# Kernel tuning notes

Hardware: AMD Instinct MI355X
Metric: run time of the kernel (lower is better)

Reference implementation:

```python
import jax, jax.numpy as jnp
import numpy as np

D_MODEL = 1024
D_HIDDEN = 4096
D_OUT = 1024
N_EXPERTS = 8
TOP_K = 2
LOAD_BALANCE_WEIGHT = 0.01


def setup_inputs() -> dict:
    key = jax.random.key(0)
    ks = jax.random.split(key, 8)
    s = 0.02
    return {
        "input_tensor": jax.random.normal(ks[0], (4, 2048, D_MODEL), dtype=jnp.float32),
        "router_w": jax.random.normal(ks[1], (N_EXPERTS, D_MODEL), dtype=jnp.float32) * s,
        "router_b": jnp.zeros((N_EXPERTS,), dtype=jnp.float32),
        "w1": jax.random.normal(ks[2], (N_EXPERTS, D_HIDDEN, D_MODEL), dtype=jnp.float32) * s,
        "b1": jnp.zeros((N_EXPERTS, D_HIDDEN), dtype=jnp.float32),
        "w2": jax.random.normal(ks[3], (N_EXPERTS, D_OUT, D_HIDDEN), dtype=jnp.float32) * s,
        "b2": jnp.zeros((N_EXPERTS, D_OUT), dtype=jnp.float32),
    }


def _moe(input_tensor, router_w, router_b, w1, b1, w2, b2):
    B, S, D = input_tensor.shape
    x = input_tensor.reshape(-1, D)  # [T, D]
    T = x.shape[0]

    router_logits = x @ router_w.T + router_b          # [T, E]
    router_probs = jax.nn.softmax(router_logits, -1)   # [T, E]
    topk_w, topk_idx = jax.lax.top_k(router_probs, TOP_K)  # [T, K]
    topk_w = topk_w / jnp.sum(topk_w, axis=-1, keepdims=True)

    # Dense combine weights: zero for unselected experts (same math as
    # gather/scatter loop since unselected contributions get weight 0).
    combine = jnp.zeros((T, N_EXPERTS), dtype=topk_w.dtype)
    combine = combine.at[jnp.arange(T)[:, None], topk_idx].add(topk_w)  # [T, E]

    out = jnp.zeros((T, D_OUT), dtype=x.dtype)
    for e in range(N_EXPERTS):  # fixed, small expert loop
        h = jax.nn.relu(x @ w1[e].T + b1[e])      # [T, H]
        y = h @ w2[e].T + b2[e]                   # [T, O]
        out = out + combine[:, e:e + 1] * y
    output = out.reshape(B, S, D_OUT)

    # Load-balance loss
    one_hot = jax.nn.one_hot(topk_idx, N_EXPERTS, dtype=router_probs.dtype)  # [T, K, E]
    usage_frac = jnp.sum(one_hot, axis=(0, 1)) / (T * TOP_K)                 # [E]
    mean_prob = jnp.mean(router_probs, axis=0)                               # [E]
    lb_loss = LOAD_BALANCE_WEIGHT * N_EXPERTS * jnp.sum(usage_frac * mean_prob)
    return output, lb_loss


def reference(input_tensor, router_w, router_b, w1, b1, w2, b2):
    return _moe(input_tensor, router_w, router_b, w1, b1, w2, b2)
```

## Files before the change

kernel.cpp:

```cpp
#include <hip/hip_runtime.h>

typedef unsigned short u16;
typedef __bf16 bf16x8 __attribute__((ext_vector_type(8)));
typedef float f32x4 __attribute__((ext_vector_type(4)));

#define T_TOKENS 8192
#define DM 1024
#define DH 4096
#define DO 1024
#define NE 8

#define XB_OFF   0ull
#define W1B_OFF  16777216ull
#define W2B_OFF  16777216ull
#define H_OFF    83886080ull
#define PT_OFF   218103808ull
#define PG_OFF   218169344ull
#define TI_OFF   218234880ull
#define TG_OFF   218300416ull
#define ST_OFF   218365952ull
#define YW_OFF   218370048ull
#define YW_SZ    67108864ull

typedef __attribute__((address_space(3))) void lds_void;
typedef __attribute__((address_space(1))) const void gbl_void;

__device__ __forceinline__ void gload_lds16(const void* g, void* l) {
  __builtin_amdgcn_global_load_lds((gbl_void*)g, (lds_void*)l, 16, 0, 0);
}

__device__ __forceinline__ u16 f2bf(float f) {
  union { float f; unsigned u; } a; a.f = f;
  unsigned u = a.u;
  return (u16)((u + 0x7FFFu + ((u >> 16) & 1u)) >> 16);
}

__global__ __launch_bounds__(256) void cast_f32_bf16(const float* __restrict__ src,
                                                     u16* __restrict__ dst, int n4) {
  int i = blockIdx.x * 256 + threadIdx.x;
  if (i >= n4) return;
  float4 v = ((const float4*)src)[i];
  ushort4 o;
  o.x = f2bf(v.x); o.y = f2bf(v.y); o.z = f2bf(v.z); o.w = f2bf(v.w);
  ((ushort4*)dst)[i] = o;
}

__global__ __launch_bounds__(256) void router_kernel(
    const float* __restrict__ x, const float* __restrict__ rw,
    const float* __restrict__ rb,
    int* __restrict__ tidx, float* __restrict__ tgate,
    int* __restrict__ counts, float* __restrict__ psum)
{
  __shared__ float srw[NE * DM];
  __shared__ float s_psum[NE];
  __shared__ int s_cnt[NE];

  for (int i = threadIdx.x; i < NE * DM; i += 256) srw[i] = rw[i];
  if (threadIdx.x < NE) { s_psum[threadIdx.x] = 0.f; s_cnt[threadIdx.x] = 0; }
  __syncthreads();

  const int wave = threadIdx.x >> 6;
  const int lane = threadIdx.x & 63;
  const int t = blockIdx.x * 4 + wave;

  float xv[16];
#pragma unroll
  for (int i = 0; i < 16; i++) xv[i] = x[(size_t)t * DM + i * 64 + lane];

  float logits[8];
#pragma unroll
  for (int e = 0; e < 8; e++) {
    float p = 0.f;
#pragma unroll
    for (int i = 0; i < 16; i++) p += xv[i] * srw[e * DM + i * 64 + lane];
#pragma unroll
    for (int o = 32; o > 0; o >>= 1) p += __shfl_xor(p, o, 64);
    logits[e] = p;
  }

  if (lane == 0) {
    float pe[8];
    float mx = -1e30f;
    for (int e = 0; e < 8; e++) { logits[e] += rb[e]; mx = fmaxf(mx, logits[e]); }
    float s = 0.f;
    for (int e = 0; e < 8; e++) { pe[e] = expf(logits[e] - mx); s += pe[e]; }
    float inv = 1.f / s;
    for (int e = 0; e < 8; e++) { pe[e] *= inv; atomicAdd(&s_psum[e], pe[e]); }
    int i0 = 0;
    for (int e = 1; e < 8; e++) if (pe[e] > pe[i0]) i0 = e;
    int i1 = (i0 == 0) ? 1 : 0;
    for (int e = 0; e < 8; e++) if (e != i0 && pe[e] > pe[i1]) i1 = e;
    float g = pe[i0] + pe[i1];
    tidx[t * 2] = i0; tidx[t * 2 + 1] = i1;
    tgate[t * 2] = pe[i0] / g; tgate[t * 2 + 1] = pe[i1] / g;
    atomicAdd(&s_cnt[i0], 1); atomicAdd(&s_cnt[i1], 1);
  }
  __syncthreads();
  if (threadIdx.x < NE) {
    atomicAdd(&counts[threadIdx.x], s_cnt[threadIdx.x]);
    atomicAdd(&psum[threadIdx.x], s_psum[threadIdx.x]);
  }
}

__global__ void offsets_kernel(const int* __restrict__ counts, int* __restrict__ offs) {
  if (threadIdx.x == 0) {
    int a = 0;
    for (int e = 0; e < NE; e++) { offs[e] = a; a += counts[e]; }
  }
}

__global__ __launch_bounds__(256) void scatter_kernel(
    const int* tidx, const float* __restrict__ tgate,
    const int* __restrict__ offs, int* __restrict__ cursor,
    int* __restrict__ ptok, float* __restrict__ pgate, int* ppos)
{
  int t = blockIdx.x * 256 + threadIdx.x;
  int e0 = tidx[t * 2], e1 = tidx[t * 2 + 1];
  float g0 = tgate[t * 2], g1 = tgate[t * 2 + 1];
  int p0 = offs[e0] + atomicAdd(&cursor[e0], 1);
  int p1 = offs[e1] + atomicAdd(&cursor[e1], 1);
  ptok[p0] = t; pgate[p0] = g0;
  ptok[p1] = t; pgate[p1] = g1;
  ppos[t * 2] = p0; ppos[t * 2 + 1] = p1;
}


#define FENCE asm volatile("" ::: "memory")
#define BAR  do { FENCE; __builtin_amdgcn_s_barrier(); FENCE; } while (0)
#define VMW4 asm volatile("s_waitcnt vmcnt(4)" ::: "memory")
#define VMW0 asm volatile("s_waitcnt vmcnt(0)" ::: "memory")

#define G256_DECLS                                                             \
  __shared__ __align__(16) u16 sm[65536];                         \
  const int tid = threadIdx.x;                                                 \
  const int lane = tid & 63;                                                   \
  const int wave = tid >> 6;                                                   \
  const int wm = wave & 1, wn = wave >> 1;                                     \
  const int q = lane >> 4, ml = lane & 15;                                     \
  const int swz0 = (q ^ (ml & 7)) * 8;             \
  const int swz1 = ((4 + q) ^ (ml & 7)) * 8;                   \
  const int baseA = wm * 8192 + ml * 64;                                       \
  const int baseB = 16384 + (wn >> 1) * 8192 + (wn & 1) * 4096 + ml * 64;      \
  const int cs = ((tid & 7) ^ ((tid >> 3) & 7)) * 8;    \
  const int srow = tid >> 3;          \
  f32x4 acc[8][4];                                                             \
  { const f32x4 z_ = {0.f, 0.f, 0.f, 0.f};                                     \
    _Pragma("unroll") for (int i_ = 0; i_ < 8; i_++)                           \
      _Pragma("unroll") for (int j_ = 0; j_ < 4; j_++) acc[i_][j_] = z_; }     \
  bf16x8 areg[4][2], breg[4][2];

#define STAGE_A(buf, half, k0)                                                 \
  { u16* d_ = sm + (buf) * 32768 + (half) * 8192 + tid * 8;                    \
    gload_lds16(aP[half][0] + (k0), d_);                                       \
    gload_lds16(aP[half][1] + (k0), d_ + 4096); }

#define STAGE_B(buf, half, k0, KD)                                             \
  { u16* d_ = sm + (buf) * 32768 + 16384 + (half) * 8192 + tid * 8;            \
    gload_lds16(bB + (size_t)((half) * 128) * (KD) + (k0), d_);                \
    gload_lds16(bB + (size_t)((half) * 128 + 64) * (KD) + (k0), d_ + 4096); }

#define READ_A(buf, mh)                                                        \
  _Pragma("unroll") for (int m_ = 0; m_ < 4; m_++) {                           \
    areg[m_][0] = *(const bf16x8*)&sm[(buf) * 32768 + baseA +                  \
                                      ((mh) * 4 + m_) * 1024 + swz0];          \
    areg[m_][1] = *(const bf16x8*)&sm[(buf) * 32768 + baseA +                  \
                                      ((mh) * 4 + m_) * 1024 + swz1];          \
  }

#define READ_B(buf, nh)                                                        \
  _Pragma("unroll") for (int n_ = 0; n_ < 2; n_++) {                           \
    breg[(nh) * 2 + n_][0] = *(const bf16x8*)&sm[(buf) * 32768 + baseB +       \
                                      ((nh) * 2 + n_) * 1024 + swz0];          \
    breg[(nh) * 2 + n_][1] = *(const bf16x8*)&sm[(buf) * 32768 + baseB +       \
                                      ((nh) * 2 + n_) * 1024 + swz1];          \
  }

#define MFMA_Q(mh, nh)                                                         \
  __builtin_amdgcn_s_setprio(1);                                               \
  _Pragma("unroll") for (int m_ = 0; m_ < 4; m_++)                             \
    _Pragma("unroll") for (int n_ = 0; n_ < 2; n_++) {                         \
      acc[(mh)*4+m_][(nh)*2+n_] = __builtin_amdgcn_mfma_f32_16x16x32_bf16(     \
          areg[m_][0], breg[(nh)*2+n_][0], acc[(mh)*4+m_][(nh)*2+n_], 0,0,0);  \
      acc[(mh)*4+m_][(nh)*2+n_] = __builtin_amdgcn_mfma_f32_16x16x32_bf16(     \
          areg[m_][1], breg[(nh)*2+n_][1], acc[(mh)*4+m_][(nh)*2+n_], 0,0,0);  \
    }                                                                          \
  __builtin_amdgcn_s_setprio(0);

#define G256_ITER(KD, k1, k2, k3, ST)                                          \
  READ_A(0, 0) READ_B(0, 0)                                                    \
  STAGE_A(1, 1, (k1))                                                          \
  BAR; MFMA_Q(0, 0) BAR;                                                       \
  READ_B(0, 1)                                                                 \
  STAGE_B(1, 1, (k1), KD)                                                      \
  BAR; MFMA_Q(0, 1) BAR;                                                       \
  READ_A(0, 1)                                                                 \
  if (ST) STAGE_B(0, 0, (k2), KD)                                              \
  BAR; MFMA_Q(1, 1) BAR;                                                       \
  if (ST) STAGE_A(0, 0, (k2))                                                  \
  BAR; MFMA_Q(1, 0)                                                            \
  if (ST) { VMW4; } else { VMW0; }                                             \
  BAR;                                                                         \
  READ_A(1, 0) READ_B(1, 0)                                                    \
  if (ST) STAGE_A(0, 1, (k2))                                                  \
  BAR; MFMA_Q(0, 0) BAR;                                                       \
  READ_B(1, 1)                                                                 \
  if (ST) STAGE_B(0, 1, (k2), KD)                                              \
  BAR; MFMA_Q(0, 1) BAR;                                                       \
  READ_A(1, 1)                                                                 \
  if (ST) STAGE_B(1, 0, (k3), KD)                                              \
  BAR; MFMA_Q(1, 1) BAR;                                                       \
  if (ST) STAGE_A(1, 0, (k3))                                                  \
  BAR; MFMA_Q(1, 0)                                                            \
  if (ST) { VMW4; }                                                            \
  BAR;

#define G256_KLOOP(KD)                                                         \
  STAGE_B(0, 0, 0, KD) STAGE_A(0, 0, 0)                                        \
  STAGE_A(0, 1, 0) STAGE_B(0, 1, 0, KD)                                        \
  STAGE_B(1, 0, 64, KD) STAGE_A(1, 0, 64)                                      \
  VMW4; BAR;                                                                   \
  for (int it_ = 0; it_ < (KD) / 128 - 1; ++it_) {                             \
    const int kb_ = it_ * 128;                                                 \
    G256_ITER(KD, kb_ + 64, kb_ + 128, kb_ + 192, 1)                           \
  }                                                                            \
  G256_ITER(KD, (KD) - 64, 0, 0, 0)

__global__ __launch_bounds__(512, 2) void gemm1_kernel(
    const u16* __restrict__ xb, const u16* __restrict__ w1b,
    const float* __restrict__ b1, const int* __restrict__ ptok,
    const int* __restrict__ offs, const int* __restrict__ counts,
    u16* __restrict__ h)
{
  const int e = blockIdx.z;
  const int cnt = counts[e];
  const int row0 = blockIdx.y * 256;
  if (row0 >= cnt) return;
  const int off = offs[e];
  const int col0 = blockIdx.x * 256;

  G256_DECLS

  const u16* aP[2][2];
#pragma unroll
  for (int a_ = 0; a_ < 2; a_++)
#pragma unroll
    for (int j_ = 0; j_ < 2; j_++) {
      int p = row0 + a_ * 128 + srow + j_ * 64;
      int tk = ptok[off + (p < cnt ? p : 0)];
      aP[a_][j_] = xb + (size_t)tk * DM + cs;
    }
  const u16* bB = w1b + ((size_t)e * DH + col0 + srow) * DM + cs;

  G256_KLOOP(DM)

#pragma unroll
  for (int M = 0; M < 8; M++) {
#pragma unroll
    for (int r_ = 0; r_ < 4; r_++) {
      int prow = row0 + wm * 128 + M * 16 + q * 4 + r_;
      if (prow < cnt) {
#pragma unroll
        for (int N = 0; N < 4; N++) {
          int gcol = col0 + wn * 64 + N * 16 + ml;
          float v = acc[M][N][r_] + b1[e * DH + gcol];
          h[(size_t)(off + prow) * DH + gcol] = f2bf(fmaxf(v, 0.f));
        }
      }
    }
  }
}

__global__ __launch_bounds__(512, 2) void gemm2_kernel(
    const u16* __restrict__ h, const u16* __restrict__ w2b,
    const float* __restrict__ b2, const int* __restrict__ ptok,
    const float* __restrict__ pgate,
    const int* __restrict__ offs, const int* __restrict__ counts,
    float* __restrict__ yw, float* __restrict__ out, int use_yw)
{
  const int e = blockIdx.z;
  const int cnt = counts[e];
  const int row0 = blockIdx.y * 256;
  if (row0 >= cnt) return;
  const int off = offs[e];
  const int col0 = blockIdx.x * 256;

  G256_DECLS

  const u16* aP[2][2];
#pragma unroll
  for (int a_ = 0; a_ < 2; a_++)
#pragma unroll
    for (int j_ = 0; j_ < 2; j_++) {
      int p = row0 + a_ * 128 + srow + j_ * 64;
      aP[a_][j_] = h + (size_t)(off + (p < cnt ? p : 0)) * DH + cs;
    }
  const u16* bB = w2b + ((size_t)e * DO + col0 + srow) * DH + cs;

  G256_KLOOP(DH)

#pragma unroll
  for (int M = 0; M < 8; M++) {
#pragma unroll
    for (int r_ = 0; r_ < 4; r_++) {
      int prow = row0 + wm * 128 + M * 16 + q * 4 + r_;
      if (prow < cnt) {
        int pr = off + prow;
        float g = pgate[pr];
        if (use_yw) {
#pragma unroll
          for (int N = 0; N < 4; N++) {
            int gcol = col0 + wn * 64 + N * 16 + ml;
            yw[(size_t)pr * DO + gcol] = g * (acc[M][N][r_] + b2[e * DO + gcol]);
          }
        } else {
          int t = ptok[pr];
#pragma unroll
          for (int N = 0; N < 4; N++) {
            int gcol = col0 + wn * 64 + N * 16 + ml;
            atomicAdd(&out[(size_t)t * DO + gcol], g * (acc[M][N][r_] + b2[e * DO + gcol]));
          }
        }
      }
    }
  }
}

__global__ __launch_bounds__(256) void combine_kernel(
    const float* __restrict__ yw, const int* __restrict__ ppos,
    float* __restrict__ out)
{
  int t = blockIdx.x;
  int j = threadIdx.x;
  int p0 = ppos[t * 2], p1 = ppos[t * 2 + 1];
  float4 a = ((const float4*)(yw + (size_t)p0 * DO))[j];
  float4 b = ((const float4*)(yw + (size_t)p1 * DO))[j];
  float4 o;
  o.x = a.x + b.x; o.y = a.y + b.y; o.z = a.z + b.z; o.w = a.w + b.w;
  ((float4*)(out + (size_t)t * DO))[j] = o;
}

__global__ void loss_kernel(const int* __restrict__ counts, const float* __restrict__ psum,
                            float* __restrict__ out, size_t idx, int T) {
  if (threadIdx.x == 0 && blockIdx.x == 0) {
    float s = 0.f;
    for (int e = 0; e < NE; e++)
      s += ((float)counts[e] / (float)(T * 2)) * (psum[e] / (float)T);
    out[idx] = 0.01f * 8.0f * s;
  }
}

extern "C" void kernel_launch(void* const* d_in, const int* in_sizes, int n_in,
                              void* d_out, int out_size, void* d_ws, size_t ws_size,
                              hipStream_t stream) {
  const float* x  = (const float*)d_in[0];
  const float* rw = (const float*)d_in[1];
  const float* rb = (const float*)d_in[2];
  const float* w1 = (const float*)d_in[3];
  const float* b1 = (const float*)d_in[4];
  const float* w2 = (const float*)d_in[5];
  const float* b2 = (const float*)d_in[6];
  float* out = (float*)d_out;
  char* ws = (char*)d_ws;

  u16* xb    = (u16*)(ws + XB_OFF);
  u16* w1b   = (u16*)(ws + W1B_OFF);
  u16* w2b   = (u16*)(ws + W2B_OFF);
  u16* h     = (u16*)(ws + H_OFF);
  int* ptok  = (int*)(ws + PT_OFF);
  float* pgate = (float*)(ws + PG_OFF);
  int* tidx  = (int*)(ws + TI_OFF);
  float* tgate = (float*)(ws + TG_OFF);
  int* counts = (int*)(ws + ST_OFF);
  int* cursor = (int*)(ws + ST_OFF + 32);
  int* offs   = (int*)(ws + ST_OFF + 64);
  float* psum = (float*)(ws + ST_OFF + 96);
  int* ppos   = tidx;
  float* yw   = (float*)(ws + YW_OFF);

  const bool use_yw = ws_size >= YW_OFF + YW_SZ;

  if (!use_yw)
    hipMemsetAsync(d_out, 0, (size_t)out_size * sizeof(float), stream);
  hipMemsetAsync(ws + ST_OFF, 0, 256, stream);

  cast_f32_bf16<<<(T_TOKENS * DM / 4 + 255) / 256, 256, 0, stream>>>(x, xb, T_TOKENS * DM / 4);
  cast_f32_bf16<<<(NE * DH * DM / 4 + 255) / 256, 256, 0, stream>>>(w1, w1b, NE * DH * DM / 4);

  router_kernel<<<T_TOKENS / 4, 256, 0, stream>>>(x, rw, rb, tidx, tgate, counts, psum);
  offsets_kernel<<<1, 64, 0, stream>>>(counts, offs);
  scatter_kernel<<<T_TOKENS / 256, 256, 0, stream>>>(tidx, tgate, offs, cursor, ptok, pgate, ppos);

  gemm1_kernel<<<dim3(DH / 256, 32, NE), 512, 0, stream>>>(xb, w1b, b1, ptok, offs, counts, h);

  cast_f32_bf16<<<(NE * DO * DH / 4 + 255) / 256, 256, 0, stream>>>(w2, w2b, NE * DO * DH / 4);

  gemm2_kernel<<<dim3(DO / 256, 32, NE), 512, 0, stream>>>(
      h, w2b, b2, ptok, pgate, offs, counts, yw, out, use_yw ? 1 : 0);

  if (use_yw)
    combine_kernel<<<T_TOKENS, 256, 0, stream>>>(yw, ppos, out);

  loss_kernel<<<1, 1, 0, stream>>>(counts, psum, out, (size_t)out_size - 1, T_TOKENS);
}
```

Baseline: 837.0 us.

## Fuse both expert GEMMs into a persistent kernel with per-row-tile dependency flags

Replaces the separate gemm1 and gemm2 launches with one persistent kernel of 256 blocks that pulls tiles from a global atomic counter. GEMM1 tiles are handed out first. GEMM2 tiles spin-wait on per-(expert, row-tile) completion counters, so second-layer work on finished rows can overlap with the tail of the first layer. The w2 bf16 copy moves to its own workspace region so it can be cast before the fused kernel without overwriting w1b. This removes the kernel boundary and the wave-quantization tail between the two GEMMs, at the cost of spin-waiting and a larger workspace requirement. If the workspace is too small it falls back to the original path.

```diff
diff --git a/kernel.cpp b/kernel.cpp
--- a/kernel.cpp
+++ b/kernel.cpp
@@ -19,7 +19,9 @@
 #define TI_OFF   218234880ull
 #define TG_OFF   218300416ull
 #define ST_OFF   218365952ull
-#define YW_OFF   218370048ull
+#define W2X_OFF  218370048ull
+#define W2X_SZ   67108864ull
+#define YW_OFF   285478912ull
 #define YW_SZ    67108864ull
 
 typedef __attribute__((address_space(3))) void lds_void;
@@ -130,8 +132,7 @@
 #define VMW4 asm volatile("s_waitcnt vmcnt(4)" ::: "memory")
 #define VMW0 asm volatile("s_waitcnt vmcnt(0)" ::: "memory")
 
-#define G256_DECLS                                                             \
-  __shared__ __align__(16) u16 sm[65536];                         \
+#define G256_IDS                                                               \
   const int tid = threadIdx.x;                                                 \
   const int lane = tid & 63;                                                   \
   const int wave = tid >> 6;                                                   \
@@ -142,12 +143,12 @@
   const int baseA = wm * 8192 + ml * 64;                                       \
   const int baseB = 16384 + (wn >> 1) * 8192 + (wn & 1) * 4096 + ml * 64;      \
   const int cs = ((tid & 7) ^ ((tid >> 3) & 7)) * 8;    \
-  const int srow = tid >> 3;          \
-  f32x4 acc[8][4];                                                             \
+  const int srow = tid >> 3;
+
+#define G256_ACC_ZERO                                                          \
   { const f32x4 z_ = {0.f, 0.f, 0.f, 0.f};                                     \
     _Pragma("unroll") for (int i_ = 0; i_ < 8; i_++)                           \
-      _Pragma("unroll") for (int j_ = 0; j_ < 4; j_++) acc[i_][j_] = z_; }     \
-  bf16x8 areg[4][2], breg[4][2];
+      _Pragma("unroll") for (int j_ = 0; j_ < 4; j_++) acc[i_][j_] = z_; }
 
 #define STAGE_A(buf, half, k0)                                                 \
   { u16* d_ = sm + (buf) * 32768 + (half) * 8192 + tid * 8;                    \
@@ -225,6 +226,135 @@
   }                                                                            \
   G256_ITER(KD, (KD) - 64, 0, 0, 0)
 
+__global__ __launch_bounds__(512, 2) void moe_mlp_fused(
+    const u16* __restrict__ xb, const u16* __restrict__ w1b,
+    const float* __restrict__ b1, const u16* __restrict__ w2b,
+    const float* __restrict__ b2, const int* __restrict__ ptok,
+    const float* __restrict__ pgate, const int* __restrict__ offs,
+    const int* __restrict__ counts, u16* __restrict__ hbuf,
+    float* __restrict__ yw, float* out, int* done, int* gctr, int use_yw)
+{
+  __shared__ __align__(16) u16 sm[65536];
+  __shared__ int s_tk;
+  G256_IDS
+  f32x4 acc[8][4];
+  bf16x8 areg[4][2], breg[4][2];
+
+  int rt[NE];
+  int n1 = 0, n2 = 0;
+#pragma unroll
+  for (int e_ = 0; e_ < NE; e_++) {
+    rt[e_] = (counts[e_] + 255) >> 8;
+    n1 += rt[e_] * 16;
+    n2 += rt[e_] * 4;
+  }
+
+  for (;;) {
+    __syncthreads();
+    if (tid == 0) s_tk = atomicAdd(gctr, 1);
+    __syncthreads();
+    const int tk = s_tk;
+    if (tk >= n1 + n2) break;
+
+    int e = 0, idx, ry, cx, g2;
+    if (tk < n1) {
+      g2 = 0; idx = tk;
+      while (idx >= rt[e] * 16) { idx -= rt[e] * 16; e++; }
+      ry = idx >> 4; cx = idx & 15;
+    } else {
+      g2 = 1; idx = tk - n1;
+      while (idx >= rt[e] * 4) { idx -= rt[e] * 4; e++; }
+      ry = idx >> 2; cx = idx & 3;
+    }
+    const int cnt = counts[e], off = offs[e];
+    const int row0 = ry * 256, col0 = cx * 256;
+
+    G256_ACC_ZERO
+
+    if (!g2) {
+      const u16* aP[2][2];
+#pragma unroll
+      for (int a_ = 0; a_ < 2; a_++)
+#pragma unroll
+        for (int j_ = 0; j_ < 2; j_++) {
+          int p = row0 + a_ * 128 + srow + j_ * 64;
+          int tkn = ptok[off + (p < cnt ? p : row0)];
+          aP[a_][j_] = xb + (size_t)tkn * DM + cs;
+        }
+      const u16* bB = w1b + ((size_t)e * DH + col0 + srow) * DM + cs;
+
+      G256_KLOOP(DM)
+
+#pragma unroll
+      for (int M = 0; M < 8; M++) {
+#pragma unroll
+        for (int r_ = 0; r_ < 4; r_++) {
+          int prow = row0 + wm * 128 + M * 16 + q * 4 + r_;
+          if (prow < cnt) {
+#pragma unroll
+            for (int N = 0; N < 4; N++) {
+              int gcol = col0 + wn * 64 + N * 16 + ml;
+              float v = acc[M][N][r_] + b1[e * DH + gcol];
+              hbuf[(size_t)(off + prow) * DH + gcol] = f2bf(fmaxf(v, 0.f));
+            }
+          }
+        }
+      }
+      __threadfence();
+      __syncthreads();
+      if (tid == 0) atomicAdd(&done[e * 32 + ry], 1);
+    } else {
+      if (tid == 0) {
+        while (__hip_atomic_load(&done[e * 32 + ry], __ATOMIC_ACQUIRE,
+                                 __HIP_MEMORY_SCOPE_AGENT) < 16)
+          __builtin_amdgcn_s_sleep(2);
+      }
+      __syncthreads();
+      __threadfence();
+
+      const u16* aP[2][2];
+#pragma unroll
+      for (int a_ = 0; a_ < 2; a_++)
+#pragma unroll
+        for (int j_ = 0; j_ < 2; j_++) {
+          int p = row0 + a_ * 128 + srow + j_ * 64;
+          aP[a_][j_] = hbuf + (size_t)(off + (p < cnt ? p : row0)) * DH + cs;
+        }
+      const u16* bB = w2b + ((size_t)e * DO + col0 + srow) * DH + cs;
+
+      G256_KLOOP(DH)
+
+#pragma unroll
+      for (int M = 0; M < 8; M++) {
+#pragma unroll
+        for (int r_ = 0; r_ < 4; r_++) {
+          int prow = row0 + wm * 128 + M * 16 + q * 4 + r_;
+          if (prow < cnt) {
+            int pr = off + prow;
+            float g = pgate[pr];
+            if (use_yw) {
+#pragma unroll
+              for (int N = 0; N < 4; N++) {
+                int gcol = col0 + wn * 64 + N * 16 + ml;
+                yw[(size_t)pr * DO + gcol] = g * (acc[M][N][r_] + b2[e * DO + gcol]);
+              }
+            } else {
+              int t = ptok[pr];
+#pragma unroll
+              for (int N = 0; N < 4; N++) {
+                int gcol = col0 + wn * 64 + N * 16 + ml;
+                atomicAdd(&out[(size_t)t * DO + gcol],
+                          g * (acc[M][N][r_] + b2[e * DO + gcol]));
+              }
+            }
+          }
+        }
+      }
+    }
+  }
+}
+
+
 __global__ __launch_bounds__(512, 2) void gemm1_kernel(
     const u16* __restrict__ xb, const u16* __restrict__ w1b,
     const float* __restrict__ b1, const int* __restrict__ ptok,
@@ -238,7 +368,11 @@
   const int off = offs[e];
   const int col0 = blockIdx.x * 256;
 
-  G256_DECLS
+  __shared__ __align__(16) u16 sm[65536];
+  G256_IDS
+  f32x4 acc[8][4];
+  bf16x8 areg[4][2], breg[4][2];
+  G256_ACC_ZERO
 
   const u16* aP[2][2];
 #pragma unroll
@@ -275,7 +409,7 @@
     const float* __restrict__ b2, const int* __restrict__ ptok,
     const float* __restrict__ pgate,
     const int* __restrict__ offs, const int* __restrict__ counts,
-    float* __restrict__ yw, float* __restrict__ out, int use_yw)
+    float* __restrict__ out)
 {
   const int e = blockIdx.z;
   const int cnt = counts[e];
@@ -284,7 +418,11 @@
   const int off = offs[e];
   const int col0 = blockIdx.x * 256;
 
-  G256_DECLS
+  __shared__ __align__(16) u16 sm[65536];
+  G256_IDS
+  f32x4 acc[8][4];
+  bf16x8 areg[4][2], breg[4][2];
+  G256_ACC_ZERO
 
   const u16* aP[2][2];
 #pragma unroll
@@ -306,19 +444,12 @@
       if (prow < cnt) {
         int pr = off + prow;
         float g = pgate[pr];
-        if (use_yw) {
-#pragma unroll
-          for (int N = 0; N < 4; N++) {
-            int gcol = col0 + wn * 64 + N * 16 + ml;
-            yw[(size_t)pr * DO + gcol] = g * (acc[M][N][r_] + b2[e * DO + gcol]);
-          }
-        } else {
-          int t = ptok[pr];
-#pragma unroll
-          for (int N = 0; N < 4; N++) {
-            int gcol = col0 + wn * 64 + N * 16 + ml;
-            atomicAdd(&out[(size_t)t * DO + gcol], g * (acc[M][N][r_] + b2[e * DO + gcol]));
-          }
+        int t = ptok[pr];
+#pragma unroll
+        for (int N = 0; N < 4; N++) {
+          int gcol = col0 + wn * 64 + N * 16 + ml;
+          atomicAdd(&out[(size_t)t * DO + gcol],
+                    g * (acc[M][N][r_] + b2[e * DO + gcol]));
         }
       }
     }
@@ -374,14 +505,14 @@
   int* cursor = (int*)(ws + ST_OFF + 32);
   int* offs   = (int*)(ws + ST_OFF + 64);
   float* psum = (float*)(ws + ST_OFF + 96);
+  int* done   = (int*)(ws + ST_OFF + 128);
+  int* gctr   = (int*)(ws + ST_OFF + 1152);
   int* ppos   = tidx;
-  float* yw   = (float*)(ws + YW_OFF);
-
-  const bool use_yw = ws_size >= YW_OFF + YW_SZ;
-
-  if (!use_yw)
-    hipMemsetAsync(d_out, 0, (size_t)out_size * sizeof(float), stream);
-  hipMemsetAsync(ws + ST_OFF, 0, 256, stream);
+
+  const bool fused_yw = ws_size >= YW_OFF + YW_SZ;
+  const bool fused_at = !fused_yw && ws_size >= W2X_OFF + W2X_SZ;
+
+  hipMemsetAsync(ws + ST_OFF, 0, 1280, stream);
 
   cast_f32_bf16<<<(T_TOKENS * DM / 4 + 255) / 256, 256, 0, stream>>>(x, xb, T_TOKENS * DM / 4);
   cast_f32_bf16<<<(NE * DH * DM / 4 + 255) / 256, 256, 0, stream>>>(w1, w1b, NE * DH * DM / 4);
@@ -390,15 +521,25 @@
   offsets_kernel<<<1, 64, 0, stream>>>(counts, offs);
   scatter_kernel<<<T_TOKENS / 256, 256, 0, stream>>>(tidx, tgate, offs, cursor, ptok, pgate, ppos);
 
-  gemm1_kernel<<<dim3(DH / 256, 32, NE), 512, 0, stream>>>(xb, w1b, b1, ptok, offs, counts, h);
-
-  cast_f32_bf16<<<(NE * DO * DH / 4 + 255) / 256, 256, 0, stream>>>(w2, w2b, NE * DO * DH / 4);
-
-  gemm2_kernel<<<dim3(DO / 256, 32, NE), 512, 0, stream>>>(
-      h, w2b, b2, ptok, pgate, offs, counts, yw, out, use_yw ? 1 : 0);
-
-  if (use_yw)
-    combine_kernel<<<T_TOKENS, 256, 0, stream>>>(yw, ppos, out);
+  if (fused_yw || fused_at) {
+    u16* w2x  = (u16*)(ws + W2X_OFF);
+    float* yw = fused_yw ? (float*)(ws + YW_OFF) : nullptr;
+    if (!fused_yw)
+      hipMemsetAsync(d_out, 0, (size_t)out_size * sizeof(float), stream);
+    cast_f32_bf16<<<(NE * DO * DH / 4 + 255) / 256, 256, 0, stream>>>(w2, w2x, NE * DO * DH / 4);
+
+    moe_mlp_fused<<<256, 512, 0, stream>>>(xb, w1b, b1, w2x, b2, ptok, pgate,
+                                           offs, counts, h, yw, out, done, gctr,
+                                           fused_yw ? 1 : 0);
+    if (fused_yw)
+      combine_kernel<<<T_TOKENS, 256, 0, stream>>>(yw, ppos, out);
+  } else {
+    hipMemsetAsync(d_out, 0, (size_t)out_size * sizeof(float), stream);
+    gemm1_kernel<<<dim3(DH / 256, 32, NE), 512, 0, stream>>>(xb, w1b, b1, ptok, offs, counts, h);
+    cast_f32_bf16<<<(NE * DO * DH / 4 + 255) / 256, 256, 0, stream>>>(w2, w2b, NE * DO * DH / 4);
+    gemm2_kernel<<<dim3(DO / 256, 32, NE), 512, 0, stream>>>(
+        h, w2b, b2, ptok, pgate, offs, counts, out);
+  }
 
   loss_kernel<<<1, 1, 0, stream>>>(counts, psum, out, (size_t)out_size - 1, T_TOKENS);
 }
```

Result: slower. 1.280 ms (+53.0%).
